# Performance work log

Hardware: AMD Instinct MI355X
Metric: run time of the kernel (lower is better)

## Reference

```python
import jax, jax.numpy as jnp
import numpy as np

DIM = 1024
HEADS = 16
HEAD_DIM = DIM // HEADS
MLP_HIDDEN = int(DIM * 0.7)  # 716
EPS = 1e-5


def _ln(x, g, b):
    m = jnp.mean(x, axis=-1, keepdims=True)
    v = jnp.mean(jnp.square(x - m), axis=-1, keepdims=True)
    return (x - m) * jax.lax.rsqrt(v + EPS) * g + b


def setup_inputs() -> dict:
    key = jax.random.key(0)
    ks = jax.random.split(key, 8)
    B, N = 4, 1024
    x = jax.random.normal(ks[0], (B, N, DIM), dtype=jnp.float32)
    s = 0.02
    return {
        "x": x,
        "norm_g": jnp.ones((DIM,), jnp.float32),
        "norm_b": jnp.zeros((DIM,), jnp.float32),
        "W1": jax.random.normal(ks[1], (DIM, 3 * DIM + MLP_HIDDEN), jnp.float32) * s,
        "b1": jnp.zeros((3 * DIM + MLP_HIDDEN,), jnp.float32),
        "qn_g": jnp.ones((HEAD_DIM,), jnp.float32),
        "qn_b": jnp.zeros((HEAD_DIM,), jnp.float32),
        "kn_g": jnp.ones((HEAD_DIM,), jnp.float32),
        "kn_b": jnp.zeros((HEAD_DIM,), jnp.float32),
        "projW": jax.random.normal(ks[2], (DIM, DIM), jnp.float32) * s,
        "projb": jnp.zeros((DIM,), jnp.float32),
        "mlpW": jax.random.normal(ks[3], (MLP_HIDDEN, DIM), jnp.float32) * s,  # mlp_bias=False
        "W2": jax.random.normal(ks[4], (2 * DIM, DIM), jnp.float32) * s,
        "b2": jnp.zeros((DIM,), jnp.float32),
        "ls_g": jnp.full((DIM,), 1e-5, jnp.float32),
    }


def reference(x, norm_g, norm_b, W1, b1, qn_g, qn_b, kn_g, kn_b,
              projW, projb, mlpW, W2, b2, ls_g):
    B, N, C = x.shape
    norm_x = _ln(x, norm_g, norm_b)
    f1 = norm_x @ W1 + b1  # (B, N, 3*dim + mlp_hidden)
    qkv, mlp_hidden = f1[..., :3 * DIM], f1[..., 3 * DIM:]
    # (B, N, 3, H, hd) -> (3, B, H, N, hd)
    qkv = qkv.reshape(B, N, 3, HEADS, HEAD_DIM).transpose(2, 0, 3, 1, 4)
    q, k, v = qkv[0], qkv[1], qkv[2]
    q = _ln(q, qn_g, qn_b)
    k = _ln(k, kn_g, kn_b)
    attn = jnp.einsum('bhnd,bhmd->bhnm', q, k) * (HEAD_DIM ** -0.5)
    attn = jax.nn.softmax(attn, axis=-1)
    xo = jnp.einsum('bhnm,bhmd->bhnd', attn, v)
    xo = xo.transpose(0, 2, 1, 3).reshape(B, N, DIM)
    attn_out = xo @ projW + projb
    mlp_out = jax.nn.gelu(mlp_hidden, approximate=False) @ mlpW  # no bias
    combined = jnp.concatenate([attn_out, mlp_out], axis=-1)
    out = x + (combined @ W2 + b2) * ls_g
    return out
```

## Files before the change

### kernel.cpp

```cpp
#include <hip/hip_runtime.h>
#include <cstdint>
#include <cstddef>

typedef unsigned short u16;
typedef unsigned char u8;
typedef __attribute__((ext_vector_type(8))) u16 u16x8;
typedef __attribute__((ext_vector_type(8))) __bf16 bf16x8;
typedef __attribute__((ext_vector_type(4))) float f32x4;
typedef __attribute__((ext_vector_type(16))) float f32x16;
typedef __attribute__((ext_vector_type(4))) int i32x4;
typedef __attribute__((ext_vector_type(8))) int i32x8;

__device__ __forceinline__ u16 f2bf(float f) {
  unsigned u = __builtin_bit_cast(unsigned, f);
  return (u16)((u + 0x7FFFu + ((u >> 16) & 1u)) >> 16);
}
__device__ __forceinline__ float bf2f(u16 h) {
  return __builtin_bit_cast(float, (unsigned)h << 16);
}
__device__ __forceinline__ u8 f2fp8(float f) {
  return (u8)(__builtin_amdgcn_cvt_pk_fp8_f32(f, 0.f, 0, false) & 0xFF);
}
__device__ __forceinline__ f32x4 mfma16(u16x8 a, u16x8 b, f32x4 c) {
  return __builtin_amdgcn_mfma_f32_16x16x32_bf16(
      __builtin_bit_cast(bf16x8, a), __builtin_bit_cast(bf16x8, b), c, 0, 0, 0);
}
__device__ __forceinline__ void load_lds16(const void* g, void* l) {
  __builtin_amdgcn_global_load_lds(
      (const __attribute__((address_space(1))) void*)g,
      (__attribute__((address_space(3))) void*)l, 16, 0, 0);
}

__global__ __launch_bounds__(256) void k_trcvt_all(
    const float* __restrict__ W1, const float* __restrict__ projW,
    const float* __restrict__ mlpW, const float* __restrict__ W2,
    u8* __restrict__ W1t, u8* __restrict__ pWt, u8* __restrict__ mWt,
    u8* __restrict__ W2t) {
  __shared__ float t[32][33];
  const int L = blockIdx.x;
  const float* src;
  u8* dst;
  int R, C, dR, dC, bx, by;
  if (L < 3840) {
    src = W1; dst = W1t; R = 1024; C = 3788; dR = 1024; dC = 3840;
    bx = L % 120; by = L / 120;
  } else if (L < 4864) {
    int tq = L - 3840;
    src = projW; dst = pWt; R = 1024; C = 1024; dR = 1024; dC = 1024;
    bx = tq & 31; by = tq >> 5;
  } else if (L < 5632) {
    int tq = L - 4864;
    src = mlpW; dst = mWt; R = 716; C = 1024; dR = 768; dC = 1024;
    bx = tq & 31; by = tq >> 5;
  } else {
    int tq = L - 5632;
    src = W2; dst = W2t; R = 2048; C = 1024; dR = 2048; dC = 1024;
    bx = tq & 31; by = tq >> 5;
  }
  const int n0 = bx * 32, k0 = by * 32;
  const int tx = threadIdx.x & 31, ty = threadIdx.x >> 5;
#pragma unroll
  for (int j = 0; j < 4; ++j) {
    int kk = k0 + ty + 8 * j, nn = n0 + tx;
    float v = (kk < R && nn < C) ? src[(size_t)kk * C + nn] : 0.f;
    t[ty + 8 * j][tx] = v;
  }
  __syncthreads();
#pragma unroll
  for (int j = 0; j < 4; ++j) {
    int nn = n0 + ty + 8 * j, kk = k0 + tx;
    if (nn < dC && kk < dR) dst[(size_t)nn * dR + kk] = f2fp8(t[tx][ty + 8 * j]);
  }
}

__global__ __launch_bounds__(256) void k_trvt(const u16* __restrict__ f1,
                                              u16* __restrict__ vtb) {
  __shared__ u16 t[32][33];
  const int z = blockIdx.z;
  const int b = z >> 4, h = z & 15;
  const int d0 = blockIdx.x * 32, n0 = blockIdx.y * 32;
  const int tx = threadIdx.x & 31, ty = threadIdx.x >> 5;
#pragma unroll
  for (int j = 0; j < 4; ++j)
    t[ty + 8 * j][tx] =
        f1[(size_t)(b * 1024 + n0 + ty + 8 * j) * 3840 + 2048 + h * 64 + d0 + tx];
  __syncthreads();
#pragma unroll
  for (int j = 0; j < 4; ++j)
    vtb[(size_t)z * 65536 + (size_t)(d0 + ty + 8 * j) * 1024 + n0 + tx] =
        t[tx][ty + 8 * j];
}

__global__ __launch_bounds__(256) void k_lnx(const float* __restrict__ x,
                                             const float* __restrict__ g,
                                             const float* __restrict__ b,
                                             u8* __restrict__ out) {
  const int row = blockIdx.x, tid = threadIdx.x;
  float4 v = ((const float4*)(x + (size_t)row * 1024))[tid];
  float s = v.x + v.y + v.z + v.w;
  float ss = v.x * v.x + v.y * v.y + v.z * v.z + v.w * v.w;
#pragma unroll
  for (int off = 1; off < 64; off <<= 1) {
    s += __shfl_xor(s, off);
    ss += __shfl_xor(ss, off);
  }
  __shared__ float red[8];
  const int wid = tid >> 6, lane = tid & 63;
  if (lane == 0) { red[wid] = s; red[4 + wid] = ss; }
  __syncthreads();
  s = red[0] + red[1] + red[2] + red[3];
  ss = red[4] + red[5] + red[6] + red[7];
  const float mean = s * (1.f / 1024.f);
  const float var = ss * (1.f / 1024.f) - mean * mean;
  const float rstd = rsqrtf(var + 1e-5f);
  float4 gv = ((const float4*)g)[tid];
  float4 bv = ((const float4*)b)[tid];
  float y0 = (v.x - mean) * rstd * gv.x + bv.x;
  float y1 = (v.y - mean) * rstd * gv.y + bv.y;
  float y2 = (v.z - mean) * rstd * gv.z + bv.z;
  float y3 = (v.w - mean) * rstd * gv.w + bv.w;
  int pk = __builtin_amdgcn_cvt_pk_fp8_f32(y0, y1, 0, false);
  pk = __builtin_amdgcn_cvt_pk_fp8_f32(y2, y3, pk, true);
  ((int*)(out + (size_t)row * 1024))[tid] = pk;
}

__device__ __forceinline__ void gemm_fp8_core(const u8* __restrict__ A,
                                              const u8* __restrict__ B, int K,
                                              u8* Alds, u8* Blds,
                                              f32x16 (&acc)[2][2], int tid) {
  const int lane = tid & 63, wave = tid >> 6;
  const int h = lane >> 5, r32 = lane & 31;
  const int wrow = (wave >> 1) * 64, wcol = (wave & 1) * 64;
  const int srow0 = tid >> 2, spos = tid & 3;
  const int nk = K >> 6;
  for (int kt = 0; kt < nk; ++kt) {
#pragma unroll
    for (int p = 0; p < 2; ++p) {
      const int row = p * 64 + srow0;
      const int c = spos ^ ((row >> 1) & 3);
      const size_t go = (size_t)row * K + kt * 64 + c * 16;
      load_lds16(A + go, Alds + (p * 256 + tid) * 16);
      load_lds16(B + go, Blds + (p * 256 + tid) * 16);
    }
    __syncthreads();
    i32x8 af[2], bf[2];
#pragma unroll
    for (int t = 0; t < 2; ++t) {
      {
        const int row = wrow + t * 32 + r32;
        const int sw = (row >> 1) & 3;
        i32x4 lo = *(const i32x4*)(Alds + row * 64 + ((2 * h) ^ sw) * 16);
        i32x4 hi = *(const i32x4*)(Alds + row * 64 + ((2 * h + 1) ^ sw) * 16);
        i32x8 a;
        a[0] = lo[0]; a[1] = lo[1]; a[2] = lo[2]; a[3] = lo[3];
        a[4] = hi[0]; a[5] = hi[1]; a[6] = hi[2]; a[7] = hi[3];
        af[t] = a;
      }
      {
        const int row = wcol + t * 32 + r32;
        const int sw = (row >> 1) & 3;
        i32x4 lo = *(const i32x4*)(Blds + row * 64 + ((2 * h) ^ sw) * 16);
        i32x4 hi = *(const i32x4*)(Blds + row * 64 + ((2 * h + 1) ^ sw) * 16);
        i32x8 b8;
        b8[0] = lo[0]; b8[1] = lo[1]; b8[2] = lo[2]; b8[3] = lo[3];
        b8[4] = hi[0]; b8[5] = hi[1]; b8[6] = hi[2]; b8[7] = hi[3];
        bf[t] = b8;
      }
    }
#pragma unroll
    for (int i = 0; i < 2; ++i)
#pragma unroll
      for (int j = 0; j < 2; ++j)
        acc[i][j] = __builtin_amdgcn_mfma_scale_f32_32x32x64_f8f6f4(
            af[i], bf[j], acc[i][j], 0, 0, 0, 0x7F7F7F7F, 0, 0x7F7F7F7F);
    __syncthreads();
  }
}

__device__ __forceinline__ void gemm_fp8_core64(const u8* __restrict__ A,
                                                const u8* __restrict__ B, int K,
                                                u8* Alds, u8* Blds,
                                                f32x16 (&acc)[2], int tid) {
  const int lane = tid & 63, wave = tid >> 6;
  const int h = lane >> 5, r32 = lane & 31;
  const int wrow = (wave >> 1) * 32, wcol = (wave & 1) * 64;
  const int nk = K >> 6;
  for (int kt = 0; kt < nk; ++kt) {
    {
      const int r = tid >> 2, pos = tid & 3;
      const int c = pos ^ ((r >> 1) & 3);
      load_lds16(A + (size_t)r * K + kt * 64 + c * 16, Alds + tid * 16);
    }
#pragma unroll
    for (int p = 0; p < 2; ++p) {
      const int s = tid + 256 * p;
      const int r = s >> 2, pos = s & 3;
      const int c = pos ^ ((r >> 1) & 3);
      load_lds16(B + (size_t)r * K + kt * 64 + c * 16, Blds + s * 16);
    }
    __syncthreads();
    i32x8 af, bf[2];
    {
      const int row = wrow + r32;
      const int sw = (row >> 1) & 3;
      i32x4 lo = *(const i32x4*)(Alds + row * 64 + ((2 * h) ^ sw) * 16);
      i32x4 hi = *(const i32x4*)(Alds + row * 64 + ((2 * h + 1) ^ sw) * 16);
      af[0] = lo[0]; af[1] = lo[1]; af[2] = lo[2]; af[3] = lo[3];
      af[4] = hi[0]; af[5] = hi[1]; af[6] = hi[2]; af[7] = hi[3];
    }
#pragma unroll
    for (int t = 0; t < 2; ++t) {
      const int row = wcol + t * 32 + r32;
      const int sw = (row >> 1) & 3;
      i32x4 lo = *(const i32x4*)(Blds + row * 64 + ((2 * h) ^ sw) * 16);
      i32x4 hi = *(const i32x4*)(Blds + row * 64 + ((2 * h + 1) ^ sw) * 16);
      i32x8 b8;
      b8[0] = lo[0]; b8[1] = lo[1]; b8[2] = lo[2]; b8[3] = lo[3];
      b8[4] = hi[0]; b8[5] = hi[1]; b8[6] = hi[2]; b8[7] = hi[3];
      bf[t] = b8;
    }
#pragma unroll
    for (int j = 0; j < 2; ++j)
      acc[j] = __builtin_amdgcn_mfma_scale_f32_32x32x64_f8f6f4(
          af, bf[j], acc[j], 0, 0, 0, 0x7F7F7F7F, 0, 0x7F7F7F7F);
    __syncthreads();
  }
}

__global__ __launch_bounds__(256) void k_gemm1(const u8* __restrict__ nx8,
                                               const u8* __restrict__ W1t,
                                               u16* __restrict__ f1,
                                               const float* __restrict__ b1) {
  __shared__ __align__(16) u8 Alds[128 * 64];
  __shared__ __align__(16) u8 Blds[128 * 64];
  const int tid = threadIdx.x, bm = blockIdx.y, bn = blockIdx.x;
  f32x16 acc[2][2];
#pragma unroll
  for (int i = 0; i < 2; ++i)
#pragma unroll
    for (int j = 0; j < 2; ++j)
#pragma unroll
      for (int r = 0; r < 16; ++r) acc[i][j][r] = 0.f;
  gemm_fp8_core(nx8 + (size_t)bm * 128 * 1024, W1t + (size_t)bn * 128 * 1024, 1024,
                Alds, Blds, acc, tid);
  const int lane = tid & 63, wave = tid >> 6;
  const int h = lane >> 5, r32 = lane & 31;
  const int wrow = (wave >> 1) * 64, wcol = (wave & 1) * 64;
#pragma unroll
  for (int i = 0; i < 2; ++i)
#pragma unroll
    for (int j = 0; j < 2; ++j) {
      const int col = bn * 128 + wcol + j * 32 + r32;
      const float bs = (col < 3788) ? b1[col] : 0.f;
#pragma unroll
      for (int r = 0; r < 16; ++r) {
        const int row = bm * 128 + wrow + i * 32 + 4 * h + (r & 3) + 8 * (r >> 2);
        f1[(size_t)row * 3840 + col] = f2bf(acc[i][j][r] + bs);
      }
    }
}

__global__ __launch_bounds__(256) void k_gemm_pm(
    const u8* __restrict__ xo, const u8* __restrict__ pWt,
    const u8* __restrict__ gel, const u8* __restrict__ mWt,
    u8* __restrict__ comb, const float* __restrict__ projb) {
  __shared__ __align__(16) u8 Alds[64 * 64];
  __shared__ __align__(16) u8 Blds[128 * 64];
  const int tid = threadIdx.x, bm = blockIdx.y, bnq = blockIdx.x;
  const u8* A;
  const u8* B;
  int K, colbase;
  const float* bias;
  if (bnq < 8) {
    A = xo + (size_t)bm * 64 * 1024;
    B = pWt + (size_t)bnq * 128 * 1024;
    K = 1024; colbase = bnq * 128; bias = projb;
  } else {
    A = gel + (size_t)bm * 64 * 768;
    B = mWt + (size_t)(bnq - 8) * 128 * 768;
    K = 768; colbase = 1024 + (bnq - 8) * 128; bias = nullptr;
  }
  f32x16 acc[2];
#pragma unroll
  for (int j = 0; j < 2; ++j)
#pragma unroll
    for (int r = 0; r < 16; ++r) acc[j][r] = 0.f;
  gemm_fp8_core64(A, B, K, Alds, Blds, acc, tid);
  const int lane = tid & 63, wave = tid >> 6;
  const int h = lane >> 5, r32 = lane & 31;
  const int wrow = (wave >> 1) * 32, wcol = (wave & 1) * 64;
#pragma unroll
  for (int j = 0; j < 2; ++j) {
    const int col = colbase + wcol + j * 32 + r32;
    const float bs = (bias != nullptr) ? bias[col] : 0.f;
#pragma unroll
    for (int r = 0; r < 16; ++r) {
      const int row = bm * 64 + wrow + 4 * h + (r & 3) + 8 * (r >> 2);
      comb[(size_t)row * 2048 + col] = f2fp8(acc[j][r] + bs);
    }
  }
}

__global__ __launch_bounds__(256) void k_gemm_fin(const u8* __restrict__ comb,
                                                  const u8* __restrict__ W2t,
                                                  float* __restrict__ out,
                                                  const float* __restrict__ b2,
                                                  const float* __restrict__ x,
                                                  const float* __restrict__ lsg) {
  __shared__ __align__(16) u8 Alds[64 * 64];
  __shared__ __align__(16) u8 Blds[128 * 64];
  const int tid = threadIdx.x, bm = blockIdx.y, bn = blockIdx.x;
  f32x16 acc[2];
#pragma unroll
  for (int j = 0; j < 2; ++j)
#pragma unroll
    for (int r = 0; r < 16; ++r) acc[j][r] = 0.f;
  gemm_fp8_core64(comb + (size_t)bm * 64 * 2048, W2t + (size_t)bn * 128 * 2048, 2048,
                  Alds, Blds, acc, tid);
  const int lane = tid & 63, wave = tid >> 6;
  const int h = lane >> 5, r32 = lane & 31;
  const int wrow = (wave >> 1) * 32, wcol = (wave & 1) * 64;
#pragma unroll
  for (int j = 0; j < 2; ++j) {
    const int col = bn * 128 + wcol + j * 32 + r32;
    const float bs = b2[col], ls = lsg[col];
#pragma unroll
    for (int r = 0; r < 16; ++r) {
      const int row = bm * 64 + wrow + 4 * h + (r & 3) + 8 * (r >> 2);
      out[(size_t)row * 1024 + col] =
          x[(size_t)row * 1024 + col] + (acc[j][r] + bs) * ls;
    }
  }
}

__global__ __launch_bounds__(256) void k_qkvgelu(const u16* __restrict__ f1,
                                                 const float* __restrict__ qg,
                                                 const float* __restrict__ qbb,
                                                 const float* __restrict__ kg,
                                                 const float* __restrict__ kbb,
                                                 u16* __restrict__ q,
                                                 u16* __restrict__ k,
                                                 u8* __restrict__ gel) {
  const int tid = threadIdx.x;
  if (blockIdx.x < 4096) {
    const int row = blockIdx.x;
    const int rem = tid >> 3;
    const int which = rem >> 4, h = rem & 15;
    const int e8 = (tid & 7) * 8;
    u16x8 xv = *(const u16x8*)(f1 + (size_t)row * 3840 + which * 1024 + h * 64 + e8);
    float xf[8];
    float s1 = 0.f, s2 = 0.f;
#pragma unroll
    for (int e = 0; e < 8; ++e) {
      xf[e] = bf2f(xv[e]);
      s1 += xf[e];
      s2 += xf[e] * xf[e];
    }
#pragma unroll
    for (int off = 1; off < 8; off <<= 1) {
      s1 += __shfl_xor(s1, off);
      s2 += __shfl_xor(s2, off);
    }
    const float mean = s1 * (1.f / 64.f);
    const float var = s2 * (1.f / 64.f) - mean * mean;
    const float rstd = rsqrtf(var + 1e-5f);
    const float* g = (which == 0) ? qg : kg;
    const float* bb = (which == 0) ? qbb : kbb;
    float4 g0 = ((const float4*)g)[e8 >> 2], g1 = ((const float4*)g)[(e8 >> 2) + 1];
    float4 b0 = ((const float4*)bb)[e8 >> 2], b1 = ((const float4*)bb)[(e8 >> 2) + 1];
    float gv[8] = {g0.x, g0.y, g0.z, g0.w, g1.x, g1.y, g1.z, g1.w};
    float bv[8] = {b0.x, b0.y, b0.z, b0.w, b1.x, b1.y, b1.z, b1.w};
    u16x8 o;
#pragma unroll
    for (int e = 0; e < 8; ++e) o[e] = f2bf((xf[e] - mean) * rstd * gv[e] + bv[e]);
    const int b = row >> 10, n = row & 1023;
    u16* dst = (which == 0) ? q : k;
    *(u16x8*)(dst + ((size_t)(b * 16 + h) * 1024 + n) * 64 + e8) = o;
  } else {
    const int id = (blockIdx.x - 4096) * 256 + tid;
    const int row = id / 96, c8 = id - row * 96;
    u16x8 xv = *(const u16x8*)(f1 + (size_t)row * 3840 + 3072 + c8 * 8);
    float rr[8];
#pragma unroll
    for (int e = 0; e < 8; ++e) {
      const int col = c8 * 8 + e;
      rr[e] = 0.f;
      if (col < 716) {
        float xx = bf2f(xv[e]);
        rr[e] = 0.5f * xx * (1.f + erff(xx * 0.70710678118654752f));
      }
    }
    int p0 = __builtin_amdgcn_cvt_pk_fp8_f32(rr[0], rr[1], 0, false);
    p0 = __builtin_amdgcn_cvt_pk_fp8_f32(rr[2], rr[3], p0, true);
    int p1 = __builtin_amdgcn_cvt_pk_fp8_f32(rr[4], rr[5], 0, false);
    p1 = __builtin_amdgcn_cvt_pk_fp8_f32(rr[6], rr[7], p1, true);
    uint2 pk;
    pk.x = (unsigned)p0;
    pk.y = (unsigned)p1;
    *(uint2*)(gel + (size_t)row * 768 + c8 * 8) = pk;
  }
}

__global__ __launch_bounds__(256) void k_flash(const u16* __restrict__ q,
                                               const u16* __restrict__ k,
                                               const u16* __restrict__ vt,
                                               u8* __restrict__ xo) {
  __shared__ __align__(16) u16 Kl[2][64 * 64];
  __shared__ __align__(16) u16 Vl[2][64 * 64];
  __shared__ __align__(16) u16 Pl[4 * 16 * 64];
  const int tid = threadIdx.x, wave = tid >> 6, lane = tid & 63;
  const int l15 = lane & 15, quad = lane >> 4;
  const int L = blockIdx.x;
  const int xcd = L & 7, i = L >> 3;
  const int bh = xcd * 8 + (i & 7), qt = i >> 3;
  const int qrow0 = qt * 64 + wave * 16;
  const u16* qb = q + ((size_t)bh * 1024 + qrow0) * 64;
  const u16* kb = k + (size_t)bh * 1024 * 64;
  const u16* vb = vt + (size_t)bh * 64 * 1024;
  u16* Pw = Pl + wave * 16 * 64;

  u16x8 qf[2];
#pragma unroll
  for (int kk = 0; kk < 2; ++kk)
    qf[kk] = *(const u16x8*)(qb + (size_t)l15 * 64 + (kk * 4 + quad) * 8);

  f32x4 O[4];
  float lacc[4] = {0.f, 0.f, 0.f, 0.f};
#pragma unroll
  for (int dt = 0; dt < 4; ++dt) O[dt] = f32x4{0.f, 0.f, 0.f, 0.f};

  const int pl7 = l15 & 7;
  const int r0 = tid >> 3, c0 = (tid & 7) ^ (r0 & 7);
  const int s1 = tid + 256;
  const int r1 = s1 >> 3, c1 = (s1 & 7) ^ (r1 & 7);

  load_lds16(kb + (size_t)r0 * 64 + c0 * 8, (u16*)Kl[0] + tid * 8);
  load_lds16(kb + (size_t)r1 * 64 + c1 * 8, (u16*)Kl[0] + s1 * 8);
  load_lds16(vb + (size_t)r0 * 1024 + c0 * 8, (u16*)Vl[0] + tid * 8);
  load_lds16(vb + (size_t)r1 * 1024 + c1 * 8, (u16*)Vl[0] + s1 * 8);
  __syncthreads();

  for (int kv = 0; kv < 16; ++kv) {
    const int cur = kv & 1;
    if (kv < 15) {
      const size_t ko = (size_t)(kv + 1) * 64;
      load_lds16(kb + (ko + r0) * 64 + c0 * 8, (u16*)Kl[cur ^ 1] + tid * 8);
      load_lds16(kb + (ko + r1) * 64 + c1 * 8, (u16*)Kl[cur ^ 1] + s1 * 8);
      load_lds16(vb + (size_t)r0 * 1024 + ko + c0 * 8, (u16*)Vl[cur ^ 1] + tid * 8);
      load_lds16(vb + (size_t)r1 * 1024 + ko + c1 * 8, (u16*)Vl[cur ^ 1] + s1 * 8);
    }
    const u16* Kc = (const u16*)Kl[cur];
    const u16* Vc = (const u16*)Vl[cur];
    f32x4 S[4];
#pragma unroll
    for (int j = 0; j < 4; ++j) S[j] = f32x4{0.f, 0.f, 0.f, 0.f};
    __builtin_amdgcn_s_setprio(1);
#pragma unroll
    for (int j = 0; j < 4; ++j)
#pragma unroll
      for (int kk = 0; kk < 2; ++kk) {
        const int pos = (kk * 4 + quad) ^ pl7;
        u16x8 bfr = *(const u16x8*)(Kc + (16 * j + l15) * 64 + pos * 8);
        S[j] = mfma16(qf[kk], bfr, S[j]);
      }
    __builtin_amdgcn_s_setprio(0);
#pragma unroll
    for (int j = 0; j < 4; ++j)
#pragma unroll
      for (int r = 0; r < 4; ++r) {
        float pv = __expf(S[j][r] * 0.125f);
        lacc[r] += pv;
        const int prow = quad * 4 + r;
        const int pc = 2 * j + (l15 >> 3);
        Pw[prow * 64 + (pc ^ (prow & 7)) * 8 + pl7] = f2bf(pv);
      }
    __builtin_amdgcn_s_waitcnt(0xC07F);
    __builtin_amdgcn_s_setprio(1);
#pragma unroll
    for (int c = 0; c < 2; ++c) {
      const int pos = (c * 4 + quad) ^ pl7;
      u16x8 pa = *(const u16x8*)(Pw + l15 * 64 + pos * 8);
#pragma unroll
      for (int dt = 0; dt < 4; ++dt) {
        u16x8 vf = *(const u16x8*)(Vc + (16 * dt + l15) * 64 + pos * 8);
        O[dt] = mfma16(pa, vf, O[dt]);
      }
    }
    __builtin_amdgcn_s_setprio(0);
    __syncthreads();
  }
#pragma unroll
  for (int r = 0; r < 4; ++r) {
#pragma unroll
    for (int off = 1; off < 16; off <<= 1) lacc[r] += __shfl_xor(lacc[r], off);
  }
  const int b = bh >> 4, h = bh & 15;
#pragma unroll
  for (int r = 0; r < 4; ++r) {
    const float inv = 1.f / lacc[r];
    u8* orow = xo + (size_t)(b * 1024 + qrow0 + quad * 4 + r) * 1024 + h * 64;
#pragma unroll
    for (int dt = 0; dt < 4; ++dt) orow[16 * dt + l15] = f2fp8(O[dt][r] * inv);
  }
}

extern "C" void kernel_launch(void* const* d_in, const int* in_sizes, int n_in,
                              void* d_out, int out_size, void* d_ws, size_t ws_size,
                              hipStream_t stream) {
  (void)in_sizes; (void)n_in; (void)out_size; (void)ws_size;
  const float* x      = (const float*)d_in[0];
  const float* norm_g = (const float*)d_in[1];
  const float* norm_b = (const float*)d_in[2];
  const float* W1     = (const float*)d_in[3];
  const float* b1     = (const float*)d_in[4];
  const float* qn_g   = (const float*)d_in[5];
  const float* qn_b   = (const float*)d_in[6];
  const float* kn_g   = (const float*)d_in[7];
  const float* kn_b   = (const float*)d_in[8];
  const float* projW  = (const float*)d_in[9];
  const float* projb  = (const float*)d_in[10];
  const float* mlpW   = (const float*)d_in[11];
  const float* W2     = (const float*)d_in[12];
  const float* b2     = (const float*)d_in[13];
  const float* ls_g   = (const float*)d_in[14];

  char* ws = (char*)d_ws;
  u8*  W1t8 = (u8*)(ws + 0);
  u8*  pWt8 = (u8*)(ws + 3932160);
  u8*  mWt8 = (u8*)(ws + 4980736);
  u8*  W2t8 = (u8*)(ws + 5767168);
  u8*  nx8  = (u8*)(ws + 7864320);
  u16* f1   = (u16*)(ws + 12058624);
  u16* qbuf = (u16*)(ws + 43515904);
  u16* kbuf = (u16*)(ws + 51904512);
  u16* vtb  = (u16*)(ws + 60293120);
  u8*  gel8 = (u8*)(ws + 68681728);

  k_trcvt_all<<<7680, 256, 0, stream>>>(W1, projW, mlpW, W2, W1t8, pWt8, mWt8, W2t8);
  k_lnx<<<4096, 256, 0, stream>>>(x, norm_g, norm_b, nx8);
  k_gemm1<<<dim3(30, 32), 256, 0, stream>>>(nx8, W1t8, f1, b1);
  k_qkvgelu<<<5632, 256, 0, stream>>>(f1, qn_g, qn_b, kn_g, kn_b, qbuf, kbuf, gel8);
  k_trvt<<<dim3(2, 32, 64), 256, 0, stream>>>(f1, vtb);
  k_flash<<<1024, 256, 0, stream>>>(qbuf, kbuf, vtb, nx8);
  k_gemm_pm<<<dim3(16, 64), 256, 0, stream>>>(nx8, pWt8, gel8, mWt8, (u8*)f1, projb);
  k_gemm_fin<<<dim3(8, 64), 256, 0, stream>>>((u8*)f1, W2t8, (float*)d_out, b2, x,
                                              ls_g);
}
```

Before: 233.0 us.

## Double-buffer FP8 GEMM LDS tiles and merge small elementwise kernels

Gives the FP8 GEMM cores two LDS buffers so the async global-to-LDS loads for the next K tile are issued while the current tile is fed to MFMA, and doubles the shared-memory arrays to match. Separately, the weight transpose/convert kernel and the input LayerNorm kernel are combined into one launch, and the V-transpose kernel is folded into the q/k-norm/GELU kernel, cutting two launches. The loop still ends with a barrier each iteration. The larger LDS footprint may lower occupancy.

Result: no change. 230.9 us (-0.9%).

```diff
diff --git a/kernel.cpp b/kernel.cpp
--- a/kernel.cpp
+++ b/kernel.cpp
@@ -31,97 +31,79 @@
       (__attribute__((address_space(3))) void*)l, 16, 0, 0);
 }
 
-__global__ __launch_bounds__(256) void k_trcvt_all(
+__global__ __launch_bounds__(256) void k_pre(
     const float* __restrict__ W1, const float* __restrict__ projW,
     const float* __restrict__ mlpW, const float* __restrict__ W2,
     u8* __restrict__ W1t, u8* __restrict__ pWt, u8* __restrict__ mWt,
-    u8* __restrict__ W2t) {
+    u8* __restrict__ W2t, const float* __restrict__ x,
+    const float* __restrict__ g, const float* __restrict__ b,
+    u8* __restrict__ nx8) {
   __shared__ float t[32][33];
+  __shared__ float red[8];
   const int L = blockIdx.x;
-  const float* src;
-  u8* dst;
-  int R, C, dR, dC, bx, by;
-  if (L < 3840) {
-    src = W1; dst = W1t; R = 1024; C = 3788; dR = 1024; dC = 3840;
-    bx = L % 120; by = L / 120;
-  } else if (L < 4864) {
-    int tq = L - 3840;
-    src = projW; dst = pWt; R = 1024; C = 1024; dR = 1024; dC = 1024;
-    bx = tq & 31; by = tq >> 5;
-  } else if (L < 5632) {
-    int tq = L - 4864;
-    src = mlpW; dst = mWt; R = 716; C = 1024; dR = 768; dC = 1024;
-    bx = tq & 31; by = tq >> 5;
+  const int tid = threadIdx.x;
+  if (L < 7680) {
+    const float* src;
+    u8* dst;
+    int R, C, dR, dC, bx, by;
+    if (L < 3840) {
+      src = W1; dst = W1t; R = 1024; C = 3788; dR = 1024; dC = 3840;
+      bx = L % 120; by = L / 120;
+    } else if (L < 4864) {
+      int tq = L - 3840;
+      src = projW; dst = pWt; R = 1024; C = 1024; dR = 1024; dC = 1024;
+      bx = tq & 31; by = tq >> 5;
+    } else if (L < 5632) {
+      int tq = L - 4864;
+      src = mlpW; dst = mWt; R = 716; C = 1024; dR = 768; dC = 1024;
+      bx = tq & 31; by = tq >> 5;
+    } else {
+      int tq = L - 5632;
+      src = W2; dst = W2t; R = 2048; C = 1024; dR = 2048; dC = 1024;
+      bx = tq & 31; by = tq >> 5;
+    }
+    const int n0 = bx * 32, k0 = by * 32;
+    const int tx = tid & 31, ty = tid >> 5;
+#pragma unroll
+    for (int j = 0; j < 4; ++j) {
+      int kk = k0 + ty + 8 * j, nn = n0 + tx;
+      float v = (kk < R && nn < C) ? src[(size_t)kk * C + nn] : 0.f;
+      t[ty + 8 * j][tx] = v;
+    }
+    __syncthreads();
+#pragma unroll
+    for (int j = 0; j < 4; ++j) {
+      int nn = n0 + ty + 8 * j, kk = k0 + tx;
+      if (nn < dC && kk < dR) dst[(size_t)nn * dR + kk] = f2fp8(t[tx][ty + 8 * j]);
+    }
   } else {
-    int tq = L - 5632;
-    src = W2; dst = W2t; R = 2048; C = 1024; dR = 2048; dC = 1024;
-    bx = tq & 31; by = tq >> 5;
-  }
-  const int n0 = bx * 32, k0 = by * 32;
-  const int tx = threadIdx.x & 31, ty = threadIdx.x >> 5;
-#pragma unroll
-  for (int j = 0; j < 4; ++j) {
-    int kk = k0 + ty + 8 * j, nn = n0 + tx;
-    float v = (kk < R && nn < C) ? src[(size_t)kk * C + nn] : 0.f;
-    t[ty + 8 * j][tx] = v;
-  }
-  __syncthreads();
-#pragma unroll
-  for (int j = 0; j < 4; ++j) {
-    int nn = n0 + ty + 8 * j, kk = k0 + tx;
-    if (nn < dC && kk < dR) dst[(size_t)nn * dR + kk] = f2fp8(t[tx][ty + 8 * j]);
-  }
-}
-
-__global__ __launch_bounds__(256) void k_trvt(const u16* __restrict__ f1,
-                                              u16* __restrict__ vtb) {
-  __shared__ u16 t[32][33];
-  const int z = blockIdx.z;
-  const int b = z >> 4, h = z & 15;
-  const int d0 = blockIdx.x * 32, n0 = blockIdx.y * 32;
-  const int tx = threadIdx.x & 31, ty = threadIdx.x >> 5;
-#pragma unroll
-  for (int j = 0; j < 4; ++j)
-    t[ty + 8 * j][tx] =
-        f1[(size_t)(b * 1024 + n0 + ty + 8 * j) * 3840 + 2048 + h * 64 + d0 + tx];
-  __syncthreads();
-#pragma unroll
-  for (int j = 0; j < 4; ++j)
-    vtb[(size_t)z * 65536 + (size_t)(d0 + ty + 8 * j) * 1024 + n0 + tx] =
-        t[tx][ty + 8 * j];
-}
-
-__global__ __launch_bounds__(256) void k_lnx(const float* __restrict__ x,
-                                             const float* __restrict__ g,
-                                             const float* __restrict__ b,
-                                             u8* __restrict__ out) {
-  const int row = blockIdx.x, tid = threadIdx.x;
-  float4 v = ((const float4*)(x + (size_t)row * 1024))[tid];
-  float s = v.x + v.y + v.z + v.w;
-  float ss = v.x * v.x + v.y * v.y + v.z * v.z + v.w * v.w;
-#pragma unroll
-  for (int off = 1; off < 64; off <<= 1) {
-    s += __shfl_xor(s, off);
-    ss += __shfl_xor(ss, off);
-  }
-  __shared__ float red[8];
-  const int wid = tid >> 6, lane = tid & 63;
-  if (lane == 0) { red[wid] = s; red[4 + wid] = ss; }
-  __syncthreads();
-  s = red[0] + red[1] + red[2] + red[3];
-  ss = red[4] + red[5] + red[6] + red[7];
-  const float mean = s * (1.f / 1024.f);
-  const float var = ss * (1.f / 1024.f) - mean * mean;
-  const float rstd = rsqrtf(var + 1e-5f);
-  float4 gv = ((const float4*)g)[tid];
-  float4 bv = ((const float4*)b)[tid];
-  float y0 = (v.x - mean) * rstd * gv.x + bv.x;
-  float y1 = (v.y - mean) * rstd * gv.y + bv.y;
-  float y2 = (v.z - mean) * rstd * gv.z + bv.z;
-  float y3 = (v.w - mean) * rstd * gv.w + bv.w;
-  int pk = __builtin_amdgcn_cvt_pk_fp8_f32(y0, y1, 0, false);
-  pk = __builtin_amdgcn_cvt_pk_fp8_f32(y2, y3, pk, true);
-  ((int*)(out + (size_t)row * 1024))[tid] = pk;
+    const int row = L - 7680;
+    float4 v = ((const float4*)(x + (size_t)row * 1024))[tid];
+    float s = v.x + v.y + v.z + v.w;
+    float ss = v.x * v.x + v.y * v.y + v.z * v.z + v.w * v.w;
+#pragma unroll
+    for (int off = 1; off < 64; off <<= 1) {
+      s += __shfl_xor(s, off);
+      ss += __shfl_xor(ss, off);
+    }
+    const int wid = tid >> 6, lane = tid & 63;
+    if (lane == 0) { red[wid] = s; red[4 + wid] = ss; }
+    __syncthreads();
+    s = red[0] + red[1] + red[2] + red[3];
+    ss = red[4] + red[5] + red[6] + red[7];
+    const float mean = s * (1.f / 1024.f);
+    const float var = ss * (1.f / 1024.f) - mean * mean;
+    const float rstd = rsqrtf(var + 1e-5f);
+    float4 gv = ((const float4*)g)[tid];
+    float4 bv = ((const float4*)b)[tid];
+    float y0 = (v.x - mean) * rstd * gv.x + bv.x;
+    float y1 = (v.y - mean) * rstd * gv.y + bv.y;
+    float y2 = (v.z - mean) * rstd * gv.z + bv.z;
+    float y3 = (v.w - mean) * rstd * gv.w + bv.w;
+    int pk = __builtin_amdgcn_cvt_pk_fp8_f32(y0, y1, 0, false);
+    pk = __builtin_amdgcn_cvt_pk_fp8_f32(y2, y3, pk, true);
+    ((int*)(nx8 + (size_t)row * 1024))[tid] = pk;
+  }
 }
 
 __device__ __forceinline__ void gemm_fp8_core(const u8* __restrict__ A,
@@ -133,24 +115,39 @@
   const int wrow = (wave >> 1) * 64, wcol = (wave & 1) * 64;
   const int srow0 = tid >> 2, spos = tid & 3;
   const int nk = K >> 6;
+#pragma unroll
+  for (int p = 0; p < 2; ++p) {
+    const int row = p * 64 + srow0;
+    const int c = spos ^ ((row >> 1) & 3);
+    const size_t go = (size_t)row * K + c * 16;
+    load_lds16(A + go, Alds + (p * 256 + tid) * 16);
+    load_lds16(B + go, Blds + (p * 256 + tid) * 16);
+  }
+  __syncthreads();
   for (int kt = 0; kt < nk; ++kt) {
-#pragma unroll
-    for (int p = 0; p < 2; ++p) {
-      const int row = p * 64 + srow0;
-      const int c = spos ^ ((row >> 1) & 3);
-      const size_t go = (size_t)row * K + kt * 64 + c * 16;
-      load_lds16(A + go, Alds + (p * 256 + tid) * 16);
-      load_lds16(B + go, Blds + (p * 256 + tid) * 16);
-    }
-    __syncthreads();
+    const int cur = kt & 1;
+    const u8* Ac = Alds + cur * 8192;
+    const u8* Bc = Blds + cur * 8192;
+    if (kt + 1 < nk) {
+      u8* An = Alds + (cur ^ 1) * 8192;
+      u8* Bn = Blds + (cur ^ 1) * 8192;
+#pragma unroll
+      for (int p = 0; p < 2; ++p) {
+        const int row = p * 64 + srow0;
+        const int c = spos ^ ((row >> 1) & 3);
+        const size_t go = (size_t)row * K + (size_t)(kt + 1) * 64 + c * 16;
+        load_lds16(A + go, An + (p * 256 + tid) * 16);
+        load_lds16(B + go, Bn + (p * 256 + tid) * 16);
+      }
+    }
     i32x8 af[2], bf[2];
 #pragma unroll
     for (int t = 0; t < 2; ++t) {
       {
         const int row = wrow + t * 32 + r32;
         const int sw = (row >> 1) & 3;
-        i32x4 lo = *(const i32x4*)(Alds + row * 64 + ((2 * h) ^ sw) * 16);
-        i32x4 hi = *(const i32x4*)(Alds + row * 64 + ((2 * h + 1) ^ sw) * 16);
+        i32x4 lo = *(const i32x4*)(Ac + row * 64 + ((2 * h) ^ sw) * 16);
+        i32x4 hi = *(const i32x4*)(Ac + row * 64 + ((2 * h + 1) ^ sw) * 16);
         i32x8 a;
         a[0] = lo[0]; a[1] = lo[1]; a[2] = lo[2]; a[3] = lo[3];
         a[4] = hi[0]; a[5] = hi[1]; a[6] = hi[2]; a[7] = hi[3];
@@ -159,8 +156,8 @@
       {
         const int row = wcol + t * 32 + r32;
         const int sw = (row >> 1) & 3;
-        i32x4 lo = *(const i32x4*)(Blds + row * 64 + ((2 * h) ^ sw) * 16);
-        i32x4 hi = *(const i32x4*)(Blds + row * 64 + ((2 * h + 1) ^ sw) * 16);
+        i32x4 lo = *(const i32x4*)(Bc + row * 64 + ((2 * h) ^ sw) * 16);
+        i32x4 hi = *(const i32x4*)(Bc + row * 64 + ((2 * h + 1) ^ sw) * 16);
         i32x8 b8;
         b8[0] = lo[0]; b8[1] = lo[1]; b8[2] = lo[2]; b8[3] = lo[3];
         b8[4] = hi[0]; b8[5] = hi[1]; b8[6] = hi[2]; b8[7] = hi[3];
@@ -185,26 +182,40 @@
   const int h = lane >> 5, r32 = lane & 31;
   const int wrow = (wave >> 1) * 32, wcol = (wave & 1) * 64;
   const int nk = K >> 6;
+  const int ra = tid >> 2, posa = tid & 3;
+  const int ca = posa ^ ((ra >> 1) & 3);
+  load_lds16(A + (size_t)ra * K + ca * 16, Alds + tid * 16);
+#pragma unroll
+  for (int p = 0; p < 2; ++p) {
+    const int s = tid + 256 * p;
+    const int r = s >> 2, pos = s & 3;
+    const int c = pos ^ ((r >> 1) & 3);
+    load_lds16(B + (size_t)r * K + c * 16, Blds + s * 16);
+  }
+  __syncthreads();
   for (int kt = 0; kt < nk; ++kt) {
-    {
-      const int r = tid >> 2, pos = tid & 3;
-      const int c = pos ^ ((r >> 1) & 3);
-      load_lds16(A + (size_t)r * K + kt * 64 + c * 16, Alds + tid * 16);
-    }
-#pragma unroll
-    for (int p = 0; p < 2; ++p) {
-      const int s = tid + 256 * p;
-      const int r = s >> 2, pos = s & 3;
-      const int c = pos ^ ((r >> 1) & 3);
-      load_lds16(B + (size_t)r * K + kt * 64 + c * 16, Blds + s * 16);
-    }
-    __syncthreads();
+    const int cur = kt & 1;
+    const u8* Ac = Alds + cur * 4096;
+    const u8* Bc = Blds + cur * 8192;
+    if (kt + 1 < nk) {
+      u8* An = Alds + (cur ^ 1) * 4096;
+      u8* Bn = Blds + (cur ^ 1) * 8192;
+      const size_t k1 = (size_t)(kt + 1) * 64;
+      load_lds16(A + (size_t)ra * K + k1 + ca * 16, An + tid * 16);
+#pragma unroll
+      for (int p = 0; p < 2; ++p) {
+        const int s = tid + 256 * p;
+        const int r = s >> 2, pos = s & 3;
+        const int c = pos ^ ((r >> 1) & 3);
+        load_lds16(B + (size_t)r * K + k1 + c * 16, Bn + s * 16);
+      }
+    }
     i32x8 af, bf[2];
     {
       const int row = wrow + r32;
       const int sw = (row >> 1) & 3;
-      i32x4 lo = *(const i32x4*)(Alds + row * 64 + ((2 * h) ^ sw) * 16);
-      i32x4 hi = *(const i32x4*)(Alds + row * 64 + ((2 * h + 1) ^ sw) * 16);
+      i32x4 lo = *(const i32x4*)(Ac + row * 64 + ((2 * h) ^ sw) * 16);
+      i32x4 hi = *(const i32x4*)(Ac + row * 64 + ((2 * h + 1) ^ sw) * 16);
       af[0] = lo[0]; af[1] = lo[1]; af[2] = lo[2]; af[3] = lo[3];
       af[4] = hi[0]; af[5] = hi[1]; af[6] = hi[2]; af[7] = hi[3];
     }
@@ -212,8 +223,8 @@
     for (int t = 0; t < 2; ++t) {
       const int row = wcol + t * 32 + r32;
       const int sw = (row >> 1) & 3;
-      i32x4 lo = *(const i32x4*)(Blds + row * 64 + ((2 * h) ^ sw) * 16);
-      i32x4 hi = *(const i32x4*)(Blds + row * 64 + ((2 * h + 1) ^ sw) * 16);
+      i32x4 lo = *(const i32x4*)(Bc + row * 64 + ((2 * h) ^ sw) * 16);
+      i32x4 hi = *(const i32x4*)(Bc + row * 64 + ((2 * h + 1) ^ sw) * 16);
       i32x8 b8;
       b8[0] = lo[0]; b8[1] = lo[1]; b8[2] = lo[2]; b8[3] = lo[3];
       b8[4] = hi[0]; b8[5] = hi[1]; b8[6] = hi[2]; b8[7] = hi[3];
@@ -231,8 +242,8 @@
                                                const u8* __restrict__ W1t,
                                                u16* __restrict__ f1,
                                                const float* __restrict__ b1) {
-  __shared__ __align__(16) u8 Alds[128 * 64];
-  __shared__ __align__(16) u8 Blds[128 * 64];
+  __shared__ __align__(16) u8 Alds[2 * 128 * 64];
+  __shared__ __align__(16) u8 Blds[2 * 128 * 64];
   const int tid = threadIdx.x, bm = blockIdx.y, bn = blockIdx.x;
   f32x16 acc[2][2];
 #pragma unroll
@@ -264,8 +275,8 @@
     const u8* __restrict__ xo, const u8* __restrict__ pWt,
     const u8* __restrict__ gel, const u8* __restrict__ mWt,
     u8* __restrict__ comb, const float* __restrict__ projb) {
-  __shared__ __align__(16) u8 Alds[64 * 64];
-  __shared__ __align__(16) u8 Blds[128 * 64];
+  __shared__ __align__(16) u8 Alds[2 * 64 * 64];
+  __shared__ __align__(16) u8 Blds[2 * 128 * 64];
   const int tid = threadIdx.x, bm = blockIdx.y, bnq = blockIdx.x;
   const u8* A;
   const u8* B;
@@ -307,8 +318,8 @@
                                                   const float* __restrict__ b2,
                                                   const float* __restrict__ x,
                                                   const float* __restrict__ lsg) {
-  __shared__ __align__(16) u8 Alds[64 * 64];
-  __shared__ __align__(16) u8 Blds[128 * 64];
+  __shared__ __align__(16) u8 Alds[2 * 64 * 64];
+  __shared__ __align__(16) u8 Blds[2 * 128 * 64];
   const int tid = threadIdx.x, bm = blockIdx.y, bn = blockIdx.x;
   f32x16 acc[2];
 #pragma unroll
@@ -333,17 +344,20 @@
   }
 }
 
-__global__ __launch_bounds__(256) void k_qkvgelu(const u16* __restrict__ f1,
-                                                 const float* __restrict__ qg,
-                                                 const float* __restrict__ qbb,
-                                                 const float* __restrict__ kg,
-                                                 const float* __restrict__ kbb,
-                                                 u16* __restrict__ q,
-                                                 u16* __restrict__ k,
-                                                 u8* __restrict__ gel) {
+__global__ __launch_bounds__(256) void k_mid(const u16* __restrict__ f1,
+                                             const float* __restrict__ qg,
+                                             const float* __restrict__ qbb,
+                                             const float* __restrict__ kg,
+                                             const float* __restrict__ kbb,
+                                             u16* __restrict__ q,
+                                             u16* __restrict__ k,
+                                             u8* __restrict__ gel,
+                                             u16* __restrict__ vtb) {
+  __shared__ u16 tt[32][33];
   const int tid = threadIdx.x;
-  if (blockIdx.x < 4096) {
-    const int row = blockIdx.x;
+  const int L = blockIdx.x;
+  if (L < 4096) {
+    const int row = L;
     const int rem = tid >> 3;
     const int which = rem >> 4, h = rem & 15;
     const int e8 = (tid & 7) * 8;
@@ -376,8 +390,8 @@
     const int b = row >> 10, n = row & 1023;
     u16* dst = (which == 0) ? q : k;
     *(u16x8*)(dst + ((size_t)(b * 16 + h) * 1024 + n) * 64 + e8) = o;
-  } else {
-    const int id = (blockIdx.x - 4096) * 256 + tid;
+  } else if (L < 5632) {
+    const int id = (L - 4096) * 256 + tid;
     const int row = id / 96, c8 = id - row * 96;
     u16x8 xv = *(const u16x8*)(f1 + (size_t)row * 3840 + 3072 + c8 * 8);
     float rr[8];
@@ -398,6 +412,21 @@
     pk.x = (unsigned)p0;
     pk.y = (unsigned)p1;
     *(uint2*)(gel + (size_t)row * 768 + c8 * 8) = pk;
+  } else {
+    const int t = L - 5632;
+    const int xq = t & 1, yq = (t >> 1) & 31, z = t >> 6;
+    const int b = z >> 4, h = z & 15;
+    const int d0 = xq * 32, n0 = yq * 32;
+    const int tx = tid & 31, ty = tid >> 5;
+#pragma unroll
+    for (int j = 0; j < 4; ++j)
+      tt[ty + 8 * j][tx] =
+          f1[(size_t)(b * 1024 + n0 + ty + 8 * j) * 3840 + 2048 + h * 64 + d0 + tx];
+    __syncthreads();
+#pragma unroll
+    for (int j = 0; j < 4; ++j)
+      vtb[(size_t)z * 65536 + (size_t)(d0 + ty + 8 * j) * 1024 + n0 + tx] =
+          tt[tx][ty + 8 * j];
   }
 }
 
@@ -536,11 +565,11 @@
   u16* vtb  = (u16*)(ws + 60293120);
   u8*  gel8 = (u8*)(ws + 68681728);
 
-  k_trcvt_all<<<7680, 256, 0, stream>>>(W1, projW, mlpW, W2, W1t8, pWt8, mWt8, W2t8);
-  k_lnx<<<4096, 256, 0, stream>>>(x, norm_g, norm_b, nx8);
+  k_pre<<<11776, 256, 0, stream>>>(W1, projW, mlpW, W2, W1t8, pWt8, mWt8, W2t8,
+                                   x, norm_g, norm_b, nx8);
   k_gemm1<<<dim3(30, 32), 256, 0, stream>>>(nx8, W1t8, f1, b1);
-  k_qkvgelu<<<5632, 256, 0, stream>>>(f1, qn_g, qn_b, kn_g, kn_b, qbuf, kbuf, gel8);
-  k_trvt<<<dim3(2, 32, 64), 256, 0, stream>>>(f1, vtb);
+  k_mid<<<9728, 256, 0, stream>>>(f1, qn_g, qn_b, kn_g, kn_b, qbuf, kbuf, gel8,
+                                  vtb);
   k_flash<<<1024, 256, 0, stream>>>(qbuf, kbuf, vtb, nx8);
   k_gemm_pm<<<dim3(16, 64), 256, 0, stream>>>(nx8, pWt8, gel8, mWt8, (u8*)f1, projb);
   k_gemm_fin<<<dim3(8, 64), 256, 0, stream>>>((u8*)f1, W2t8, (float*)d_out, b2, x,
```
